# Kernel optimization log

Measured on AMD Instinct MI355X. Metric: run time of the kernel, lower is better.

Reference implementation:

```python
import jax, jax.numpy as jnp
import numpy as np

EPS = 1e-05
DILATION = 1

def setup_inputs() -> dict:
    key = jax.random.key(0)
    k1, k2 = jax.random.split(key)
    B, T, D, K = 4, 4096, 2048, 4
    x = jax.random.normal(k1, (B, T, D), dtype=jnp.float32)
    norm_weight = jnp.ones((D,), dtype=jnp.float32)
    conv_weight = jax.random.normal(k2, (D, 1, K), dtype=jnp.float32) * (1.0 / np.sqrt(K))
    return {"x": x, "norm_weight": norm_weight, "conv_weight": conv_weight}

def reference(x, norm_weight, conv_weight):
    B, T, D = x.shape
    K = conv_weight.shape[-1]
    pad = (K - 1) * DILATION
    # RMSNorm over last dim
    ms = jnp.mean(jnp.square(x), axis=-1, keepdims=True)
    y = x * jax.lax.rsqrt(ms + EPS) * norm_weight
    # to channel-first [B, D, T]
    y = jnp.transpose(y, (0, 2, 1))
    # causal depthwise conv: left-pad (K-1)*dilation, valid conv == torch pad-both + slice[:T]
    y = jax.lax.conv_general_dilated(
        y, conv_weight,
        window_strides=(1,),
        padding=[(pad, 0)],
        rhs_dilation=(DILATION,),
        dimension_numbers=("NCH", "OIH", "NCH"),
        feature_group_count=D,
    )
    # SiLU then back to [B, T, D]
    y = y * jax.nn.sigmoid(y)
    return jnp.transpose(y, (0, 2, 1))
```

## Files before the change

### kernel.cpp

```cpp
#include <hip/hip_runtime.h>
#include <math.h>

#define D_DIM 2048
#define T_DIM 4096
#define K_DIM 4
#define TT    16
#define NROW  (TT + 3)
#define NTHREADS (D_DIM / 4)
#define NWAVES  (NTHREADS / 64)

__global__ __launch_bounds__(NTHREADS) void fused_kernel(
    const float* __restrict__ x,
    const float* __restrict__ g,
    const float* __restrict__ w,
    float* __restrict__ out)
{
    const int b    = blockIdx.y;
    const int t0   = blockIdx.x * TT;
    const int tid  = threadIdx.x;
    const int d0   = tid * 4;
    const int lane = tid & 63;
    const int wid  = tid >> 6;

    __shared__ float s_part[NROW][NWAVES];
    __shared__ float s_inv[NROW];

    const float* xb = x + ((size_t)b * T_DIM) * D_DIM + d0;

    float4 xv[NROW];
#pragma unroll
    for (int r = 0; r < NROW; ++r) {
        const int t = t0 - 3 + r;
        if (t >= 0) {
            xv[r] = *(const float4*)(xb + (size_t)t * D_DIM);
        } else {
            xv[r] = make_float4(0.f, 0.f, 0.f, 0.f);
        }
    }
#pragma unroll
    for (int r = 0; r < NROW; ++r) {
        float p = xv[r].x * xv[r].x + xv[r].y * xv[r].y +
                  xv[r].z * xv[r].z + xv[r].w * xv[r].w;
#pragma unroll
        for (int off = 32; off > 0; off >>= 1) p += __shfl_down(p, off, 64);
        if (lane == 0) s_part[r][wid] = p;
    }
    __syncthreads();
    if (tid < NROW) {
        float s = 0.f;
#pragma unroll
        for (int wv = 0; wv < NWAVES; ++wv) s += s_part[tid][wv];
        s_inv[tid] = rsqrtf(s * (1.0f / D_DIM) + 1e-5f);
    }
    __syncthreads();

    const float4 gv = *(const float4*)(g + d0);
#pragma unroll
    for (int r = 0; r < NROW; ++r) {
        const float rv = s_inv[r];
        xv[r].x *= rv * gv.x;
        xv[r].y *= rv * gv.y;
        xv[r].z *= rv * gv.z;
        xv[r].w *= rv * gv.w;
    }

    float wgt[4][4];
#pragma unroll
    for (int j = 0; j < 4; ++j) {
        float4 wv = *(const float4*)(w + (size_t)(d0 + j) * K_DIM);
        wgt[j][0] = wv.x; wgt[j][1] = wv.y; wgt[j][2] = wv.z; wgt[j][3] = wv.w;
    }

    float* ob = out + ((size_t)b * T_DIM) * D_DIM + d0;
#pragma unroll
    for (int i = 0; i < TT; ++i) {
        float4 o;
        float* op = &o.x;
#pragma unroll
        for (int j = 0; j < 4; ++j) {
            const float v = wgt[j][0] * ((const float*)&xv[i    ])[j]
                          + wgt[j][1] * ((const float*)&xv[i + 1])[j]
                          + wgt[j][2] * ((const float*)&xv[i + 2])[j]
                          + wgt[j][3] * ((const float*)&xv[i + 3])[j];
            op[j] = v * __builtin_amdgcn_rcpf(1.f + __expf(-v));
        }
        *(float4*)(ob + (size_t)(t0 + i) * D_DIM) = o;
    }
}

extern "C" void kernel_launch(void* const* d_in, const int* in_sizes, int n_in,
                              void* d_out, int out_size, void* d_ws, size_t ws_size,
                              hipStream_t stream) {
    const float* x = (const float*)d_in[0];
    const float* g = (const float*)d_in[1];
    const float* w = (const float*)d_in[2];
    float* out = (float*)d_out;

    const int total = in_sizes[0];
    const int rows  = total / D_DIM;
    const int B     = rows / T_DIM;

    dim3 grid(T_DIM / TT, B);
    fused_kernel<<<grid, NTHREADS, 0, stream>>>(x, g, w, out);
}
```

Baseline: 241.1 us.

## Stream rows through a double-buffered pipeline with prefetch and nontemporal stores

The kernel no longer loads all 19 rows into registers up front. It now processes two timesteps per iteration, keeps a sliding 3-row window of normalized values, and prefetches the next rows while the current pair's reduction and conv run. Per-wave partial sums go through double-buffered shared memory with one barrier per pair, outputs use nontemporal stores, and launch bounds request 4 blocks per SM. This is meant to cut register pressure so occupancy rises, and to overlap loads with compute. The cost is 8 barriers per block instead of 2, and the prefetch depth may be too shallow to hide memory latency.

```diff
diff --git a/kernel.cpp b/kernel.cpp
--- a/kernel.cpp
+++ b/kernel.cpp
@@ -3,13 +3,36 @@
 
 #define D_DIM 2048
 #define T_DIM 4096
-#define K_DIM 4
 #define TT    16
-#define NROW  (TT + 3)
-#define NTHREADS (D_DIM / 4)
-#define NWAVES  (NTHREADS / 64)
+#define NT    (D_DIM / 4)
+#define NW    (NT / 64)
 
-__global__ __launch_bounds__(NTHREADS) void fused_kernel(
+typedef float vfloat4 __attribute__((ext_vector_type(4)));
+
+__device__ __forceinline__ float row_partial(float4 v) {
+    float p = v.x * v.x + v.y * v.y + v.z * v.z + v.w * v.w;
+#pragma unroll
+    for (int off = 32; off > 0; off >>= 1) p += __shfl_down(p, off, 64);
+    return p;
+}
+
+__device__ __forceinline__ float inv_from(const float* sp) {
+    float4 a = *(const float4*)sp;
+    float4 b = *(const float4*)(sp + 4);
+    float s = a.x + a.y + a.z + a.w + b.x + b.y + b.z + b.w;
+    return rsqrtf(s * (1.0f / D_DIM) + 1e-5f);
+}
+
+__device__ __forceinline__ float silu(float v) {
+    return v * __builtin_amdgcn_rcpf(1.f + __expf(-v));
+}
+
+__device__ __forceinline__ void nt_store4(float* p, float a, float b, float c, float d) {
+    vfloat4 v = { a, b, c, d };
+    __builtin_nontemporal_store(v, (vfloat4*)p);
+}
+
+__global__ __launch_bounds__(NT, 4) void fused_kernel(
     const float* __restrict__ x,
     const float* __restrict__ g,
     const float* __restrict__ w,
@@ -22,69 +45,93 @@
     const int lane = tid & 63;
     const int wid  = tid >> 6;
 
-    __shared__ float s_part[NROW][NWAVES];
-    __shared__ float s_inv[NROW];
+    __shared__ __align__(16) float hpart[3][NW];
+    __shared__ __align__(16) float part[2][2][NW];
 
-    const float* xb = x + ((size_t)b * T_DIM) * D_DIM + d0;
+    const float* xb = x   + (size_t)b * T_DIM * D_DIM + d0;
+    float*       ob = out + (size_t)b * T_DIM * D_DIM + d0;
 
-    float4 xv[NROW];
+    float4 hv[3];
 #pragma unroll
-    for (int r = 0; r < NROW; ++r) {
+    for (int r = 0; r < 3; ++r) {
         const int t = t0 - 3 + r;
-        if (t >= 0) {
-            xv[r] = *(const float4*)(xb + (size_t)t * D_DIM);
-        } else {
-            xv[r] = make_float4(0.f, 0.f, 0.f, 0.f);
-        }
+        hv[r] = (t >= 0) ? *(const float4*)(xb + (size_t)t * D_DIM)
+                         : make_float4(0.f, 0.f, 0.f, 0.f);
     }
+    float4 cur0 = *(const float4*)(xb + (size_t)(t0 + 0) * D_DIM);
+    float4 cur1 = *(const float4*)(xb + (size_t)(t0 + 1) * D_DIM);
+    float4 nxt0 = *(const float4*)(xb + (size_t)(t0 + 2) * D_DIM);
+    float4 nxt1 = *(const float4*)(xb + (size_t)(t0 + 3) * D_DIM);
+
+    const float4 gv = *(const float4*)(g + d0);
+    float wgt[4][4];
 #pragma unroll
-    for (int r = 0; r < NROW; ++r) {
-        float p = xv[r].x * xv[r].x + xv[r].y * xv[r].y +
-                  xv[r].z * xv[r].z + xv[r].w * xv[r].w;
+    for (int j = 0; j < 4; ++j) {
+        float4 wv = *(const float4*)(w + (size_t)(d0 + j) * 4);
+        wgt[j][0] = wv.x; wgt[j][1] = wv.y; wgt[j][2] = wv.z; wgt[j][3] = wv.w;
+    }
+
 #pragma unroll
-        for (int off = 32; off > 0; off >>= 1) p += __shfl_down(p, off, 64);
-        if (lane == 0) s_part[r][wid] = p;
-    }
-    __syncthreads();
-    if (tid < NROW) {
-        float s = 0.f;
-#pragma unroll
-        for (int wv = 0; wv < NWAVES; ++wv) s += s_part[tid][wv];
-        s_inv[tid] = rsqrtf(s * (1.0f / D_DIM) + 1e-5f);
+    for (int r = 0; r < 3; ++r) {
+        float p = row_partial(hv[r]);
+        if (lane == 0) hpart[r][wid] = p;
     }
     __syncthreads();
 
-    const float4 gv = *(const float4*)(g + d0);
+    float win[3][4];
 #pragma unroll
-    for (int r = 0; r < NROW; ++r) {
-        const float rv = s_inv[r];
-        xv[r].x *= rv * gv.x;
-        xv[r].y *= rv * gv.y;
-        xv[r].z *= rv * gv.z;
-        xv[r].w *= rv * gv.w;
+    for (int r = 0; r < 3; ++r) {
+        const float inv = inv_from(hpart[r]);
+        win[r][0] = hv[r].x * inv * gv.x;
+        win[r][1] = hv[r].y * inv * gv.y;
+        win[r][2] = hv[r].z * inv * gv.z;
+        win[r][3] = hv[r].w * inv * gv.w;
     }
 
-    float wgt[4][4];
 #pragma unroll
-    for (int j = 0; j < 4; ++j) {
-        float4 wv = *(const float4*)(w + (size_t)(d0 + j) * K_DIM);
-        wgt[j][0] = wv.x; wgt[j][1] = wv.y; wgt[j][2] = wv.z; wgt[j][3] = wv.w;
-    }
+    for (int i = 0; i < TT; i += 2) {
+        const int slot = (i >> 1) & 1;
+        float p0 = row_partial(cur0);
+        float p1 = row_partial(cur1);
+        if (lane == 0) { part[slot][0][wid] = p0; part[slot][1][wid] = p1; }
+        __syncthreads();
 
-    float* ob = out + ((size_t)b * T_DIM) * D_DIM + d0;
-#pragma unroll
-    for (int i = 0; i < TT; ++i) {
-        float4 o;
-        float* op = &o.x;
+        float4 f0, f1;
+        if (i + 4 < TT) {
+            f0 = *(const float4*)(xb + (size_t)(t0 + i + 4) * D_DIM);
+            f1 = *(const float4*)(xb + (size_t)(t0 + i + 5) * D_DIM);
+        } else {
+            f0 = make_float4(0.f, 0.f, 0.f, 0.f);
+            f1 = f0;
+        }
+
+        const float r0 = inv_from(part[slot][0]);
+        const float r1 = inv_from(part[slot][1]);
+        const float y0[4] = { cur0.x * r0 * gv.x, cur0.y * r0 * gv.y,
+                              cur0.z * r0 * gv.z, cur0.w * r0 * gv.w };
+        const float y1[4] = { cur1.x * r1 * gv.x, cur1.y * r1 * gv.y,
+                              cur1.z * r1 * gv.z, cur1.w * r1 * gv.w };
+
+        float o0[4], o1[4];
 #pragma unroll
         for (int j = 0; j < 4; ++j) {
-            const float v = wgt[j][0] * ((const float*)&xv[i    ])[j]
-                          + wgt[j][1] * ((const float*)&xv[i + 1])[j]
-                          + wgt[j][2] * ((const float*)&xv[i + 2])[j]
-                          + wgt[j][3] * ((const float*)&xv[i + 3])[j];
-            op[j] = v * __builtin_amdgcn_rcpf(1.f + __expf(-v));
+            const float v0 = wgt[j][0] * win[0][j] + wgt[j][1] * win[1][j] +
+                             wgt[j][2] * win[2][j] + wgt[j][3] * y0[j];
+            o0[j] = silu(v0);
+            const float v1 = wgt[j][0] * win[1][j] + wgt[j][1] * win[2][j] +
+                             wgt[j][2] * y0[j]     + wgt[j][3] * y1[j];
+            o1[j] = silu(v1);
         }
-        *(float4*)(ob + (size_t)(t0 + i) * D_DIM) = o;
+        nt_store4(ob + (size_t)(t0 + i)     * D_DIM, o0[0], o0[1], o0[2], o0[3]);
+        nt_store4(ob + (size_t)(t0 + i + 1) * D_DIM, o1[0], o1[1], o1[2], o1[3]);
+
+#pragma unroll
+        for (int j = 0; j < 4; ++j) {
+            win[0][j] = win[2][j];
+            win[1][j] = y0[j];
+            win[2][j] = y1[j];
+        }
+        cur0 = nxt0; cur1 = nxt1; nxt0 = f0; nxt1 = f1;
     }
 }
 
@@ -101,5 +148,5 @@
     const int B     = rows / T_DIM;
 
     dim3 grid(T_DIM / TT, B);
-    fused_kernel<<<grid, NTHREADS, 0, stream>>>(x, g, w, out);
+    fused_kernel<<<grid, NT, 0, stream>>>(x, g, w, out);
 }
```

Result: no change. 239.2 us (-0.8%).
